# Performance work log

Measured on AMD Instinct MI355X. Metric: run time of the kernel, lower is better.

Reference implementation:

```python
import jax, jax.numpy as jnp
import numpy as np

B, V, N, C = 32, 5, 196, 768
H = 768          # hidden_dim of score MLP
NUM_ITERS = 3


def setup_inputs() -> dict:
    key = jax.random.key(0)
    ks = jax.random.split(key, 6)
    scale = 1.0 / np.sqrt(C)
    x = jax.random.normal(ks[0], (B, V, N, C), dtype=jnp.float32)
    # per-view projection weights, stacked: [V, C, C] (no bias)
    w_views = jax.random.uniform(ks[1], (V, C, C), dtype=jnp.float32, minval=-scale, maxval=scale)
    # score MLP: Linear(2C -> H), Tanh, Linear(H -> 1)
    s1 = 1.0 / np.sqrt(2 * C)
    w1 = jax.random.uniform(ks[2], (2 * C, H), dtype=jnp.float32, minval=-s1, maxval=s1)
    b1 = jax.random.uniform(ks[3], (H,), dtype=jnp.float32, minval=-s1, maxval=s1)
    s2 = 1.0 / np.sqrt(H)
    w2 = jax.random.uniform(ks[4], (H, 1), dtype=jnp.float32, minval=-s2, maxval=s2)
    b2 = jax.random.uniform(ks[5], (1,), dtype=jnp.float32, minval=-s2, maxval=s2)
    return {"x": x, "w_views": w_views, "w1": w1, "b1": b1, "w2": w2, "b2": b2}


def reference(x, w_views, w1, b1, w2, b2):
    # x: [B, V, N, C]
    c = x.mean(axis=1)                                   # [B, N, C]
    # per-view projections are independent of c: compute once (same math)
    proj_x = jnp.einsum('bvnc,vcd->bvnd', x, w_views)    # [B, V, N, C]
    a = None
    for _ in range(NUM_ITERS):
        c_exp = jnp.broadcast_to(c[:, None], x.shape)    # [B, V, N, C]
        si = jnp.concatenate([x, c_exp], axis=-1)        # [B, V, N, 2C]
        h = jnp.tanh(jnp.einsum('bvnk,kh->bvnh', si, w1) + b1)
        s = (jnp.einsum('bvnh,ho->bvno', h, w2) + b2)[..., 0]  # [B, V, N]
        a = jax.nn.softmax(s, axis=1)                    # softmax over views
        c = jnp.einsum('bvn,bvnc->bnc', a, proj_x)       # weighted sum over V
    eps = 1e-8
    entropy = -(a * jnp.log(a + eps)).sum(axis=1)        # [B, N]
    r = 1.0 - entropy / np.log(V)
    return c, r
```

## Files before the change

kernel.cpp:

```cpp
#include <hip/hip_runtime.h>

#define CDIM   768
#define NSEQ   196
#define NVIEW  5
#define BN_TOT 6272
#define SLAB   4816896
#define WSLAB  589824

typedef __attribute__((ext_vector_type(8))) short short8;
typedef __attribute__((ext_vector_type(4))) float f32x4;

__device__ __forceinline__ float bf_lo(unsigned u) { return __uint_as_float(u << 16); }
__device__ __forceinline__ float bf_hi(unsigned u) { return __uint_as_float(u & 0xffff0000u); }
__device__ __forceinline__ unsigned short f2bf(float f) {
  unsigned u = __float_as_uint(f);
  return (unsigned short)((u + 0x7fffu + ((u >> 16) & 1u)) >> 16);
}
__device__ __forceinline__ unsigned pack2(float f0, float f1) {
  return (unsigned)f2bf(f0) | ((unsigned)f2bf(f1) << 16);
}
__device__ __forceinline__ float ftanh(float x) {
  x = fminf(fmaxf(x, -10.f), 10.f);
  float e = __expf(2.f * x);
  return (e - 1.f) / (e + 1.f);
}
__device__ __forceinline__ void async_cp16(const void* g, void* l) {
  __builtin_amdgcn_global_load_lds((const __attribute__((address_space(1))) unsigned*)g,
                                   (__attribute__((address_space(3))) unsigned*)l, 16, 0, 0);
}

__global__ __launch_bounds__(256) void k_tr(const float* __restrict__ wv,
                                            const float* __restrict__ w1,
                                            unsigned short* __restrict__ wvT,
                                            unsigned short* __restrict__ w1aT,
                                            unsigned short* __restrict__ w1bT) {
  __shared__ float tile[32][33];
  const int m = blockIdx.z;
  const float* src;
  unsigned short* dst;
  if (m < NVIEW)      { src = wv + (size_t)m * WSLAB; dst = wvT + (size_t)m * WSLAB; }
  else if (m == NVIEW){ src = w1;                     dst = w1aT; }
  else                { src = w1 + WSLAB;             dst = w1bT; }
  const int tx = threadIdx.x, ty = threadIdx.y;
  const int x0 = blockIdx.x * 32, y0 = blockIdx.y * 32;
#pragma unroll
  for (int i = 0; i < 4; ++i)
    tile[ty + i * 8][tx] = src[(size_t)(y0 + ty + i * 8) * CDIM + x0 + tx];
  __syncthreads();
#pragma unroll
  for (int i = 0; i < 4; ++i)
    dst[(size_t)(x0 + ty + i * 8) * CDIM + y0 + tx] = f2bf(tile[tx][ty + i * 8]);
}

__global__ __launch_bounds__(192) void k_cvt_mean(const float* __restrict__ x,
                                                  unsigned short* __restrict__ xb,
                                                  unsigned short* __restrict__ cb) {
  const int bn = blockIdx.x;
  const int b = bn / NSEQ, n = bn % NSEQ;
  const int h = threadIdx.x * 4;
  const float* xp = x + ((size_t)(b * NVIEW) * NSEQ + n) * CDIM + h;
  float s0 = 0, s1 = 0, s2 = 0, s3 = 0;
#pragma unroll
  for (int v = 0; v < NVIEW; ++v) {
    float4 p = *(const float4*)(xp + (size_t)v * (NSEQ * CDIM));
    s0 += p.x; s1 += p.y; s2 += p.z; s3 += p.w;
    uint2 q; q.x = pack2(p.x, p.y); q.y = pack2(p.z, p.w);
    *(uint2*)(xb + ((size_t)v * BN_TOT + bn) * CDIM + h) = q;
  }
  uint2 o;
  o.x = pack2(s0 * 0.2f, s1 * 0.2f);
  o.y = pack2(s2 * 0.2f, s3 * 0.2f);
  *(uint2*)(cb + (size_t)bn * CDIM + h) = o;
}

template <int MODE>
__global__ __launch_bounds__(512, 4) void gemm_r(const unsigned short* __restrict__ P0,
                                                 const unsigned short* __restrict__ cbp,
                                                 const unsigned short* __restrict__ wvT,
                                                 const unsigned short* __restrict__ w1aT,
                                                 const unsigned short* __restrict__ w1bT,
                                                 unsigned short* __restrict__ Q0,
                                                 unsigned short* __restrict__ Q1,
                                                 unsigned short* __restrict__ Q2) {
  extern __shared__ unsigned short ldsb[];
  constexpr int NWG = (MODE == 0) ? 1617 : 735;
  const int orig = blockIdx.x;
  const int qq = NWG >> 3, rr = NWG & 7, xcd = orig & 7, slot0 = orig >> 3;
  const int wk = (xcd < rr ? xcd * (qq + 1) : rr * (qq + 1) + (xcd - rr) * qq) + slot0;
  const int nt = wk % 3, mt = (wk / 3) % 49, z = wk / 147;

  const int t = threadIdx.x, w = t >> 6, lane = t & 63, lr = lane & 15, lq = lane >> 4;
  const int wm = ((w >> 2) & 1) * 64;
  const int wn = (w & 3) * 64;
  const int colBase = nt * 256, mrow0 = mt * 128;

  const unsigned short *A, *Bt;
  unsigned short* C;
  if (MODE == 0) {
    if (z == 10)    { A = cbp; Bt = w1bT; C = Q2; }
    else if (z < 5) { A = P0 + (size_t)z * SLAB;       Bt = wvT + (size_t)z * WSLAB; C = Q0 + (size_t)z * SLAB; }
    else            { A = P0 + (size_t)(z - 5) * SLAB; Bt = w1aT;                    C = Q1 + (size_t)(z - 5) * SLAB; }
  } else {
    A = P0 + (size_t)z * SLAB; Bt = w1bT; C = Q0 + (size_t)z * SLAB;
  }

  const int swz = ((t & 3) ^ ((t >> 3) & 3)) << 3;
  const unsigned short* gA = A  + (size_t)(mrow0 + (t >> 2)) * CDIM + swz;
  const unsigned short* gB = Bt + (size_t)(colBase + (t >> 2)) * CDIM + swz;
  const int kch = ((lq ^ ((lr >> 1) & 3)) << 3);

#define STAGE(kt, s) {                                                            \
    unsigned short* d_ = ldsb + (s) * 12288 + (w << 9);                           \
    async_cp16(gA + (kt) * 32, d_);                                               \
    async_cp16(gB + (kt) * 32, d_ + 4096);                                        \
    async_cp16(gB + (kt) * 32 + (size_t)128 * CDIM, d_ + 8192); }

  f32x4 acc[4][4] = {};

  STAGE(0, 0); STAGE(1, 1);
  asm volatile("s_waitcnt vmcnt(3)" ::: "memory");
  __builtin_amdgcn_s_barrier();

  for (int kt = 0; kt < 24; ++kt) {
    const int s = kt % 3;
    const unsigned short* bp = ldsb + s * 12288;
    if (kt < 22) STAGE(kt + 2, (kt + 2) % 3);
    short8 af[4], bf[4];
#pragma unroll
    for (int i = 0; i < 4; ++i) af[i] = *(const short8*)(bp + (wm + i * 16 + lr) * 32 + kch);
#pragma unroll
    for (int j = 0; j < 4; ++j) bf[j] = *(const short8*)(bp + 4096 + (wn + j * 16 + lr) * 32 + kch);
    __builtin_amdgcn_s_setprio(1);
#pragma unroll
    for (int i = 0; i < 4; ++i)
#pragma unroll
      for (int j = 0; j < 4; ++j)
        acc[i][j] = __builtin_amdgcn_mfma_f32_16x16x32_bf16(af[i], bf[j], acc[i][j], 0, 0, 0);
    __builtin_amdgcn_s_setprio(0);
    if (kt < 22)       { asm volatile("s_waitcnt vmcnt(3)" ::: "memory"); }
    else if (kt == 22) { asm volatile("s_waitcnt vmcnt(0)" ::: "memory"); }
    __builtin_amdgcn_s_barrier();
  }
#undef STAGE

#pragma unroll
  for (int i = 0; i < 4; ++i)
#pragma unroll
    for (int j = 0; j < 4; ++j) {
      const int gr = mrow0 + wm + i * 16 + lq * 4;
      const int gc = colBase + wn + j * 16 + lr;
      unsigned short* cp = C + (size_t)gr * CDIM + gc;
#pragma unroll
      for (int r = 0; r < 4; ++r)
        cp[(size_t)r * CDIM] = f2bf(acc[i][j][r]);
    }
}

__global__ __launch_bounds__(192) void k_iter3(const unsigned short* __restrict__ xw1b,
                                               const unsigned short* __restrict__ cw1,
                                               const unsigned short* __restrict__ pw1b,
                                               const unsigned short* __restrict__ projb,
                                               const float* __restrict__ b1,
                                               const float* __restrict__ w2,
                                               float* __restrict__ outc,
                                               float* __restrict__ outr) {
  __shared__ float red[3][NVIEW];
  __shared__ float aa[NVIEW];
  const int bn = blockIdx.x, t = threadIdx.x, wid = t >> 6, lane = t & 63;
  const int h = t * 4;
  const float4 bv = *(const float4*)(b1 + h);
  const float4 wv = *(const float4*)(w2 + h);
  float cw[4];
  { uint2 c = *(const uint2*)(cw1 + (size_t)bn * CDIM + h);
    cw[0] = bf_lo(c.x); cw[1] = bf_hi(c.x); cw[2] = bf_lo(c.y); cw[3] = bf_hi(c.y); }
  float xw[NVIEW][4], pf[NVIEW][4];
#pragma unroll
  for (int v = 0; v < NVIEW; ++v) {
    uint2 q = *(const uint2*)(xw1b + ((size_t)v * BN_TOT + bn) * CDIM + h);
    xw[v][0] = bf_lo(q.x) + bv.x; xw[v][1] = bf_hi(q.x) + bv.y;
    xw[v][2] = bf_lo(q.y) + bv.z; xw[v][3] = bf_hi(q.y) + bv.w;
    uint2 p = *(const uint2*)(pw1b + ((size_t)v * BN_TOT + bn) * CDIM + h);
    pf[v][0] = bf_lo(p.x); pf[v][1] = bf_hi(p.x);
    pf[v][2] = bf_lo(p.y); pf[v][3] = bf_hi(p.y);
  }
  for (int it = 0; it < 3; ++it) {
    float part[NVIEW];
#pragma unroll
    for (int v = 0; v < NVIEW; ++v) {
      float p;
      p = wv.x * ftanh(xw[v][0] + cw[0]);
      p = fmaf(wv.y, ftanh(xw[v][1] + cw[1]), p);
      p = fmaf(wv.z, ftanh(xw[v][2] + cw[2]), p);
      p = fmaf(wv.w, ftanh(xw[v][3] + cw[3]), p);
      part[v] = p;
    }
#pragma unroll
    for (int off = 32; off > 0; off >>= 1)
#pragma unroll
      for (int v = 0; v < NVIEW; ++v) part[v] += __shfl_down(part[v], off);
    if (lane == 0)
#pragma unroll
      for (int v = 0; v < NVIEW; ++v) red[wid][v] = part[v];
    __syncthreads();
    if (t == 0) {
      float s[NVIEW];
#pragma unroll
      for (int v = 0; v < NVIEW; ++v) s[v] = red[0][v] + red[1][v] + red[2][v];
      float m = s[0];
#pragma unroll
      for (int v = 1; v < NVIEW; ++v) m = fmaxf(m, s[v]);
      float a[NVIEW], sum = 0.f;
#pragma unroll
      for (int v = 0; v < NVIEW; ++v) { a[v] = __expf(s[v] - m); sum += a[v]; }
      const float inv = 1.f / sum;
#pragma unroll
      for (int v = 0; v < NVIEW; ++v) { a[v] *= inv; aa[v] = a[v]; }
      if (it == 2) {
        float ent = 0.f;
#pragma unroll
        for (int v = 0; v < NVIEW; ++v) ent -= a[v] * logf(a[v] + 1e-8f);
        outr[bn] = 1.f - ent * 0.6213349345596119f;
      }
    }
    __syncthreads();
    if (it < 2) {
      float n0 = 0, n1 = 0, n2 = 0, n3 = 0;
#pragma unroll
      for (int v = 0; v < NVIEW; ++v) {
        const float av = aa[v];
        n0 = fmaf(av, pf[v][0], n0); n1 = fmaf(av, pf[v][1], n1);
        n2 = fmaf(av, pf[v][2], n2); n3 = fmaf(av, pf[v][3], n3);
      }
      cw[0] = n0; cw[1] = n1; cw[2] = n2; cw[3] = n3;
    } else {
      float r0 = 0, r1 = 0, r2 = 0, r3 = 0;
#pragma unroll
      for (int v = 0; v < NVIEW; ++v) {
        const float av = aa[v];
        uint2 p = *(const uint2*)(projb + ((size_t)v * BN_TOT + bn) * CDIM + h);
        r0 = fmaf(av, bf_lo(p.x), r0); r1 = fmaf(av, bf_hi(p.x), r1);
        r2 = fmaf(av, bf_lo(p.y), r2); r3 = fmaf(av, bf_hi(p.y), r3);
      }
      float4 of; of.x = r0; of.y = r1; of.z = r2; of.w = r3;
      *(float4*)(outc + (size_t)bn * CDIM + h) = of;
    }
  }
}

extern "C" void kernel_launch(void* const* d_in, const int* in_sizes, int n_in,
                              void* d_out, int out_size, void* d_ws, size_t ws_size,
                              hipStream_t stream) {
  (void)in_sizes; (void)n_in; (void)out_size; (void)ws_size;
  const float* x  = (const float*)d_in[0];
  const float* wv = (const float*)d_in[1];
  const float* w1 = (const float*)d_in[2];
  const float* b1 = (const float*)d_in[3];
  const float* w2 = (const float*)d_in[4];

  unsigned short* ws   = (unsigned short*)d_ws;
  unsigned short* wvT  = ws;
  unsigned short* w1aT = ws + 2949120;
  unsigned short* w1bT = ws + 3538944;
  unsigned short* xb   = ws + 4128768;
  unsigned short* pw1b = ws + 4128768;
  unsigned short* projb= ws + 28213248;
  unsigned short* xw1b = ws + 52297728;
  unsigned short* cb   = ws + 76382208;
  unsigned short* cw1  = ws + 81199104;

  float* outc = (float*)d_out;
  float* outr = outc + SLAB;

  k_tr<<<dim3(24, 24, 7), dim3(32, 8), 0, stream>>>(wv, w1, wvT, w1aT, w1bT);
  k_cvt_mean<<<BN_TOT, 192, 0, stream>>>(x, xb, cb);
  gemm_r<0><<<1617, 512, 73728, stream>>>(xb, cb, wvT, w1aT, w1bT, projb, xw1b, cw1);
  gemm_r<1><<<735, 512, 73728, stream>>>(projb, nullptr, nullptr, nullptr, w1bT,
                                         pw1b, nullptr, nullptr);
  k_iter3<<<BN_TOT, 192, 0, stream>>>(xw1b, cw1, pw1b, projb, b1, w2, outc, outr);
}
```

Before: 357.2 us.

## Retile bf16 GEMMs to 256x128 four-wave blocks and fuse cast/mean into transpose kernel

The GEMM block tile changes from 128x256 with 8 waves to 256x128 with 4 waves. Each wave now computes a 128x64 sub-tile with 8x4 MFMA accumulators, for more register-level reuse of the B fragments. M is padded to 25 tiles of 256 rows, with a per-wave guard on the store. The x-to-bf16 conversion and view-mean kernel is folded into the weight-transpose launch as an extra z-slice, so one kernel launch is removed. The costs are lower occupancy (2 blocks of 256 threads per CU), higher register pressure, and some wasted work on the padded rows.

After: 390.6 us. 9.4% more time.

```diff
diff --git a/kernel.cpp b/kernel.cpp
--- a/kernel.cpp
+++ b/kernel.cpp
@@ -29,19 +29,47 @@
                                    (__attribute__((address_space(3))) unsigned*)l, 16, 0, 0);
 }
 
-__global__ __launch_bounds__(256) void k_tr(const float* __restrict__ wv,
-                                            const float* __restrict__ w1,
-                                            unsigned short* __restrict__ wvT,
-                                            unsigned short* __restrict__ w1aT,
-                                            unsigned short* __restrict__ w1bT) {
+__global__ __launch_bounds__(256) void k_tr2(const float* __restrict__ wv,
+                                             const float* __restrict__ w1,
+                                             const float* __restrict__ x,
+                                             unsigned short* __restrict__ wvT,
+                                             unsigned short* __restrict__ w1aT,
+                                             unsigned short* __restrict__ w1bT,
+                                             unsigned short* __restrict__ xb,
+                                             unsigned short* __restrict__ cb) {
+  const int m = blockIdx.z;
+  const int tx = threadIdx.x, ty = threadIdx.y, t = ty * 32 + tx;
+  if (m == 7) {
+    const int bidx = blockIdx.y * 24 + blockIdx.x;
+    if (t < 192) {
+      const int col = t * 4;
+      for (int i = 0; i < 11; ++i) {
+        const int bn = bidx * 11 + i;
+        if (bn >= BN_TOT) break;
+        const int b = bn / NSEQ, n = bn - b * NSEQ;
+        const float* xp = x + ((size_t)(b * NVIEW) * NSEQ + n) * CDIM + col;
+        float s0 = 0, s1 = 0, s2 = 0, s3 = 0;
+#pragma unroll
+        for (int v = 0; v < NVIEW; ++v) {
+          float4 p = *(const float4*)(xp + (size_t)v * (NSEQ * CDIM));
+          s0 += p.x; s1 += p.y; s2 += p.z; s3 += p.w;
+          uint2 q; q.x = pack2(p.x, p.y); q.y = pack2(p.z, p.w);
+          *(uint2*)(xb + ((size_t)v * BN_TOT + bn) * CDIM + col) = q;
+        }
+        uint2 o;
+        o.x = pack2(s0 * 0.2f, s1 * 0.2f);
+        o.y = pack2(s2 * 0.2f, s3 * 0.2f);
+        *(uint2*)(cb + (size_t)bn * CDIM + col) = o;
+      }
+    }
+    return;
+  }
   __shared__ float tile[32][33];
-  const int m = blockIdx.z;
   const float* src;
   unsigned short* dst;
   if (m < NVIEW)      { src = wv + (size_t)m * WSLAB; dst = wvT + (size_t)m * WSLAB; }
   else if (m == NVIEW){ src = w1;                     dst = w1aT; }
   else                { src = w1 + WSLAB;             dst = w1bT; }
-  const int tx = threadIdx.x, ty = threadIdx.y;
   const int x0 = blockIdx.x * 32, y0 = blockIdx.y * 32;
 #pragma unroll
   for (int i = 0; i < 4; ++i)
@@ -52,29 +80,8 @@
     dst[(size_t)(x0 + ty + i * 8) * CDIM + y0 + tx] = f2bf(tile[tx][ty + i * 8]);
 }
 
-__global__ __launch_bounds__(192) void k_cvt_mean(const float* __restrict__ x,
-                                                  unsigned short* __restrict__ xb,
-                                                  unsigned short* __restrict__ cb) {
-  const int bn = blockIdx.x;
-  const int b = bn / NSEQ, n = bn % NSEQ;
-  const int h = threadIdx.x * 4;
-  const float* xp = x + ((size_t)(b * NVIEW) * NSEQ + n) * CDIM + h;
-  float s0 = 0, s1 = 0, s2 = 0, s3 = 0;
-#pragma unroll
-  for (int v = 0; v < NVIEW; ++v) {
-    float4 p = *(const float4*)(xp + (size_t)v * (NSEQ * CDIM));
-    s0 += p.x; s1 += p.y; s2 += p.z; s3 += p.w;
-    uint2 q; q.x = pack2(p.x, p.y); q.y = pack2(p.z, p.w);
-    *(uint2*)(xb + ((size_t)v * BN_TOT + bn) * CDIM + h) = q;
-  }
-  uint2 o;
-  o.x = pack2(s0 * 0.2f, s1 * 0.2f);
-  o.y = pack2(s2 * 0.2f, s3 * 0.2f);
-  *(uint2*)(cb + (size_t)bn * CDIM + h) = o;
-}
-
 template <int MODE>
-__global__ __launch_bounds__(512, 4) void gemm_r(const unsigned short* __restrict__ P0,
+__global__ __launch_bounds__(256, 2) void gemm_w(const unsigned short* __restrict__ P0,
                                                  const unsigned short* __restrict__ cbp,
                                                  const unsigned short* __restrict__ wvT,
                                                  const unsigned short* __restrict__ w1aT,
@@ -83,16 +90,16 @@
                                                  unsigned short* __restrict__ Q1,
                                                  unsigned short* __restrict__ Q2) {
   extern __shared__ unsigned short ldsb[];
-  constexpr int NWG = (MODE == 0) ? 1617 : 735;
+  constexpr int NWG = (MODE == 0) ? 1650 : 750;
   const int orig = blockIdx.x;
   const int qq = NWG >> 3, rr = NWG & 7, xcd = orig & 7, slot0 = orig >> 3;
   const int wk = (xcd < rr ? xcd * (qq + 1) : rr * (qq + 1) + (xcd - rr) * qq) + slot0;
-  const int nt = wk % 3, mt = (wk / 3) % 49, z = wk / 147;
+  const int nt = wk % 6, mt = (wk / 6) % 25, z = wk / 150;
 
   const int t = threadIdx.x, w = t >> 6, lane = t & 63, lr = lane & 15, lq = lane >> 4;
-  const int wm = ((w >> 2) & 1) * 64;
-  const int wn = (w & 3) * 64;
-  const int colBase = nt * 256, mrow0 = mt * 128;
+  const int wm = (w >> 1) * 128;
+  const int wn = (w & 1) * 64;
+  const int colBase = nt * 128, mrow0 = mt * 256;
 
   const unsigned short *A, *Bt;
   unsigned short* C;
@@ -111,49 +118,56 @@
 
 #define STAGE(kt, s) {                                                            \
     unsigned short* d_ = ldsb + (s) * 12288 + (w << 9);                           \
-    async_cp16(gA + (kt) * 32, d_);                                               \
-    async_cp16(gB + (kt) * 32, d_ + 4096);                                        \
-    async_cp16(gB + (kt) * 32 + (size_t)128 * CDIM, d_ + 8192); }
-
-  f32x4 acc[4][4] = {};
+    const unsigned short* a_ = gA + (kt) * 32;                                    \
+    async_cp16(a_, d_);                                                           \
+    async_cp16(a_ + (size_t)64  * CDIM, d_ + 2048);                               \
+    async_cp16(a_ + (size_t)128 * CDIM, d_ + 4096);                               \
+    async_cp16(a_ + (size_t)192 * CDIM, d_ + 6144);                               \
+    const unsigned short* b_ = gB + (kt) * 32;                                    \
+    async_cp16(b_, d_ + 8192);                                                    \
+    async_cp16(b_ + (size_t)64 * CDIM, d_ + 10240); }
+
+  f32x4 acc[8][4] = {};
 
   STAGE(0, 0); STAGE(1, 1);
-  asm volatile("s_waitcnt vmcnt(3)" ::: "memory");
+  asm volatile("s_waitcnt vmcnt(6)" ::: "memory");
   __builtin_amdgcn_s_barrier();
 
   for (int kt = 0; kt < 24; ++kt) {
     const int s = kt % 3;
     const unsigned short* bp = ldsb + s * 12288;
     if (kt < 22) STAGE(kt + 2, (kt + 2) % 3);
-    short8 af[4], bf[4];
-#pragma unroll
-    for (int i = 0; i < 4; ++i) af[i] = *(const short8*)(bp + (wm + i * 16 + lr) * 32 + kch);
-#pragma unroll
-    for (int j = 0; j < 4; ++j) bf[j] = *(const short8*)(bp + 4096 + (wn + j * 16 + lr) * 32 + kch);
+    short8 af[8], bf[4];
+#pragma unroll
+    for (int i = 0; i < 8; ++i) af[i] = *(const short8*)(bp + (wm + i * 16 + lr) * 32 + kch);
+#pragma unroll
+    for (int j = 0; j < 4; ++j) bf[j] = *(const short8*)(bp + 8192 + (wn + j * 16 + lr) * 32 + kch);
     __builtin_amdgcn_s_setprio(1);
 #pragma unroll
-    for (int i = 0; i < 4; ++i)
+    for (int i = 0; i < 8; ++i)
 #pragma unroll
       for (int j = 0; j < 4; ++j)
         acc[i][j] = __builtin_amdgcn_mfma_f32_16x16x32_bf16(af[i], bf[j], acc[i][j], 0, 0, 0);
     __builtin_amdgcn_s_setprio(0);
-    if (kt < 22)       { asm volatile("s_waitcnt vmcnt(3)" ::: "memory"); }
+    if (kt < 22)       { asm volatile("s_waitcnt vmcnt(6)" ::: "memory"); }
     else if (kt == 22) { asm volatile("s_waitcnt vmcnt(0)" ::: "memory"); }
     __builtin_amdgcn_s_barrier();
   }
 #undef STAGE
 
-#pragma unroll
-  for (int i = 0; i < 4; ++i)
-#pragma unroll
-    for (int j = 0; j < 4; ++j) {
-      const int gr = mrow0 + wm + i * 16 + lq * 4;
-      const int gc = colBase + wn + j * 16 + lr;
-      unsigned short* cp = C + (size_t)gr * CDIM + gc;
-#pragma unroll
-      for (int r = 0; r < 4; ++r)
-        cp[(size_t)r * CDIM] = f2bf(acc[i][j][r]);
-    }
+  if (mrow0 + wm < BN_TOT) {
+#pragma unroll
+    for (int i = 0; i < 8; ++i)
+#pragma unroll
+      for (int j = 0; j < 4; ++j) {
+        const int gr = mrow0 + wm + i * 16 + lq * 4;
+        const int gc = colBase + wn + j * 16 + lr;
+        unsigned short* cp = C + (size_t)gr * CDIM + gc;
+#pragma unroll
+        for (int r = 0; r < 4; ++r)
+          cp[(size_t)r * CDIM] = f2bf(acc[i][j][r]);
+      }
+  }
 }
 
 __global__ __launch_bounds__(192) void k_iter3(const unsigned short* __restrict__ xw1b,
@@ -271,10 +285,9 @@
   float* outc = (float*)d_out;
   float* outr = outc + SLAB;
 
-  k_tr<<<dim3(24, 24, 7), dim3(32, 8), 0, stream>>>(wv, w1, wvT, w1aT, w1bT);
-  k_cvt_mean<<<BN_TOT, 192, 0, stream>>>(x, xb, cb);
-  gemm_r<0><<<1617, 512, 73728, stream>>>(xb, cb, wvT, w1aT, w1bT, projb, xw1b, cw1);
-  gemm_r<1><<<735, 512, 73728, stream>>>(projb, nullptr, nullptr, nullptr, w1bT,
+  k_tr2<<<dim3(24, 24, 8), dim3(32, 8), 0, stream>>>(wv, w1, x, wvT, w1aT, w1bT, xb, cb);
+  gemm_w<0><<<1650, 256, 73728, stream>>>(xb, cb, wvT, w1aT, w1bT, projb, xw1b, cw1);
+  gemm_w<1><<<750, 256, 73728, stream>>>(projb, nullptr, nullptr, nullptr, w1bT,
                                          pw1b, nullptr, nullptr);
   k_iter3<<<BN_TOT, 192, 0, stream>>>(xw1b, cw1, pw1b, projb, b1, w2, outc, outr);
 }
```

## Double-buffer LDS fragments in registers and deepen global prefetch to three stages

Applied to the files above, without the earlier changes.

Restructures the bf16 MFMA GEMM main loop. Fragments for the next k-tile are read from LDS into a second register set while MFMAs run on the current set. Global-to-LDS async copies are now issued three tiles ahead instead of two. A sched_barrier keeps the compiler from reordering the loads into the MFMA block. The aim is to hide LDS read latency and global load latency behind matrix math, at the cost of more vector registers under a 512-thread, 4-block launch bound, which risks spills or lower occupancy.

Result: slower. 592.8 us (+66.0%).

```diff
diff --git a/kernel.cpp b/kernel.cpp
--- a/kernel.cpp
+++ b/kernel.cpp
@@ -71,6 +71,23 @@
   o.x = pack2(s0 * 0.2f, s1 * 0.2f);
   o.y = pack2(s2 * 0.2f, s3 * 0.2f);
   *(uint2*)(cb + (size_t)bn * CDIM + h) = o;
+}
+
+__device__ __forceinline__ void ldfrag(const unsigned short* bp, int wm, int wn,
+                                       int lr, int kch, short8* af, short8* bf) {
+#pragma unroll
+  for (int i = 0; i < 4; ++i) af[i] = *(const short8*)(bp + (wm + i * 16 + lr) * 32 + kch);
+#pragma unroll
+  for (int j = 0; j < 4; ++j) bf[j] = *(const short8*)(bp + 4096 + (wn + j * 16 + lr) * 32 + kch);
+}
+__device__ __forceinline__ void domfma(const short8* af, const short8* bf, f32x4 acc[4][4]) {
+  __builtin_amdgcn_s_setprio(1);
+#pragma unroll
+  for (int i = 0; i < 4; ++i)
+#pragma unroll
+    for (int j = 0; j < 4; ++j)
+      acc[i][j] = __builtin_amdgcn_mfma_f32_16x16x32_bf16(af[i], bf[j], acc[i][j], 0, 0, 0);
+  __builtin_amdgcn_s_setprio(0);
 }
 
 template <int MODE>
@@ -116,31 +133,32 @@
     async_cp16(gB + (kt) * 32 + (size_t)128 * CDIM, d_ + 8192); }
 
   f32x4 acc[4][4] = {};
-
-  STAGE(0, 0); STAGE(1, 1);
+  short8 afA[4], bfA[4], afB[4], bfB[4];
+
+  STAGE(0, 0); STAGE(1, 1); STAGE(2, 2);
   asm volatile("s_waitcnt vmcnt(3)" ::: "memory");
   __builtin_amdgcn_s_barrier();
-
-  for (int kt = 0; kt < 24; ++kt) {
-    const int s = kt % 3;
-    const unsigned short* bp = ldsb + s * 12288;
-    if (kt < 22) STAGE(kt + 2, (kt + 2) % 3);
-    short8 af[4], bf[4];
-#pragma unroll
-    for (int i = 0; i < 4; ++i) af[i] = *(const short8*)(bp + (wm + i * 16 + lr) * 32 + kch);
-#pragma unroll
-    for (int j = 0; j < 4; ++j) bf[j] = *(const short8*)(bp + 4096 + (wn + j * 16 + lr) * 32 + kch);
-    __builtin_amdgcn_s_setprio(1);
-#pragma unroll
-    for (int i = 0; i < 4; ++i)
-#pragma unroll
-      for (int j = 0; j < 4; ++j)
-        acc[i][j] = __builtin_amdgcn_mfma_f32_16x16x32_bf16(af[i], bf[j], acc[i][j], 0, 0, 0);
-    __builtin_amdgcn_s_setprio(0);
-    if (kt < 22)       { asm volatile("s_waitcnt vmcnt(3)" ::: "memory"); }
-    else if (kt == 22) { asm volatile("s_waitcnt vmcnt(0)" ::: "memory"); }
-    __builtin_amdgcn_s_barrier();
-  }
+  ldfrag(ldsb, wm, wn, lr, kch, afA, bfA);
+  asm volatile("s_waitcnt lgkmcnt(0)" ::: "memory");
+  __builtin_amdgcn_s_barrier();
+
+#define PHASE(kt, afR, bfR, afW, bfW) {                                          \
+    if ((kt) < 23) ldfrag(ldsb + (((kt) + 1) % 3) * 12288, wm, wn, lr, kch,      \
+                          afW, bfW);                                             \
+    if ((kt) <= 20) STAGE((kt) + 3, (kt) % 3);                                   \
+    __builtin_amdgcn_sched_barrier(0);        \
+    domfma(afR, bfR, acc);                       \
+    if ((kt) <= 20)      { asm volatile("s_waitcnt vmcnt(3)" ::: "memory"); }    \
+    else if ((kt) == 21) { asm volatile("s_waitcnt vmcnt(0)" ::: "memory"); }    \
+    asm volatile("s_waitcnt lgkmcnt(0)" ::: "memory");                           \
+    __builtin_amdgcn_s_barrier();                                                \
+  }
+
+  for (int kt = 0; kt < 24; kt += 2) {
+    PHASE(kt,     afA, bfA, afB, bfB);
+    PHASE(kt + 1, afB, bfB, afA, bfA);
+  }
+#undef PHASE
 #undef STAGE
 
 #pragma unroll
```
